# Optimization experiments

Measured on AMD Instinct MI355X. Metric: run time of the kernel, lower is better.

The kernel has to match this reference:

```python
import jax, jax.numpy as jnp
import numpy as np

PH, CH, Z, H, W, NK = 4, 8, 8, 320, 320, 4096
ITERS, GAMMA, TAU, EPS, RATIO = 3, 0.1, 0.2, 0.01, 0.2
LO, HI = int(Z * RATIO), Z - int(Z * RATIO)  # effective_slice = slice(1, 7)
TWO_PI = 2.0 * np.pi


def to_c(x):
    return jax.lax.complex(x[..., 0], x[..., 1])


def warp(img, flow):
    # MVF motion warp. img: (PH, Z, H, W) complex; flow: (PH, 2, Z, H, W) pixel displacements.
    gy = jnp.clip(jnp.arange(H, dtype=flow.dtype)[:, None] + flow[:, 0], 0.0, H - 1.0)
    gx = jnp.clip(jnp.arange(W, dtype=flow.dtype)[None, :] + flow[:, 1], 0.0, W - 1.0)
    y0 = jnp.floor(gy); x0 = jnp.floor(gx)
    wy = gy - y0; wx = gx - x0
    y0 = y0.astype(jnp.int32); x0 = x0.astype(jnp.int32)
    y1 = jnp.minimum(y0 + 1, H - 1); x1 = jnp.minimum(x0 + 1, W - 1)
    flat = img.reshape(PH, Z, H * W)
    def g(yi, xi):
        return jnp.take_along_axis(flat, (yi * W + xi).reshape(PH, Z, H * W), axis=-1).reshape(PH, Z, H, W)
    return (g(y0, x0) * ((1 - wy) * (1 - wx)) + g(y0, x1) * ((1 - wy) * wx)
            + g(y1, x0) * (wy * (1 - wx)) + g(y1, x1) * (wy * wx))


def nufft(img, traj):
    # Type-2 NUFFT via FFT + bilinear k-space interpolation.
    # img: (PH, CH, Z, H, W) complex; traj: (PH, 2, NK) in [-pi, pi).
    F = jnp.fft.fftshift(jnp.fft.fft2(img), axes=(-2, -1))
    gy = jnp.clip((traj[:, 0] / TWO_PI + 0.5) * H, 0.0, H - 1.0)
    gx = jnp.clip((traj[:, 1] / TWO_PI + 0.5) * W, 0.0, W - 1.0)
    def samp(Fp, gyp, gxp):
        y0 = jnp.floor(gyp); x0 = jnp.floor(gxp)
        wy = gyp - y0; wx = gxp - x0
        y0 = y0.astype(jnp.int32); x0 = x0.astype(jnp.int32)
        y1 = jnp.minimum(y0 + 1, H - 1); x1 = jnp.minimum(x0 + 1, W - 1)
        return (Fp[..., y0, x0] * ((1 - wy) * (1 - wx)) + Fp[..., y0, x1] * ((1 - wy) * wx)
                + Fp[..., y1, x0] * (wy * (1 - wx)) + Fp[..., y1, x1] * (wy * wx))
    return jax.vmap(samp)(F, gy, gx)  # (PH, CH, Z, NK)


def forward_model(x, mvf, csm_c, traj):
    # A = NUFFT * CSM * MVF
    warped = warp(x, mvf)                # (PH, Z, H, W)
    coil = csm_c[None] * warped[:, None]  # (PH, CH, Z, H, W)
    return nufft(coil, traj)             # (PH, CH, Z, NK)


def tv_energy(x):
    # smooth (anisotropic) TV energy; grad_reg = std * d/dx TV(x) = x_eff - regularization(x_eff)
    dy = x[..., 1:, :] - x[..., :-1, :]
    dx = x[..., :, 1:] - x[..., :, :-1]
    return jnp.sum(jnp.sqrt(jnp.abs(dy) ** 2 + 1e-8)) + jnp.sum(jnp.sqrt(jnp.abs(dx) ** 2 + 1e-8))


def setup_inputs():
    key = jax.random.key(0)
    ks = jax.random.split(key, 6)
    kspace_data = 0.1 * jax.random.normal(ks[0], (1, PH, CH, Z, NK, 2), jnp.float32)
    kspace_traj = jax.random.uniform(ks[1], (PH, 2, NK), jnp.float32, -np.pi, np.pi)
    image_init = jax.random.normal(ks[2], (1, PH, Z, H, W, 2), jnp.float32)
    mvf = 2.0 * jax.random.normal(ks[3], (PH, 2, Z, H, W), jnp.float32)
    csm = jax.random.normal(ks[4], (CH, Z, H, W, 2), jnp.float32) / np.sqrt(CH)
    std = jax.random.uniform(ks[5], (1,), jnp.float32, 0.05, 0.15)
    return {"kspace_data": kspace_data, "kspace_traj": kspace_traj, "image_init": image_init,
            "mvf": mvf, "csm": csm, "std": std}


def reference(kspace_data, kspace_traj, image_init, mvf, csm, std):
    y = to_c(kspace_data)[0]                   # (PH, CH, Z, NK)
    x = to_c(jnp.nan_to_num(image_init))[0]     # (PH, Z, H, W)
    csm_c = to_c(csm)                           # (CH, Z, H, W)
    s = std[0]

    def dc_loss(xv):
        est = forward_model(xv, mvf, csm_c, kspace_traj)[:, :, LO:HI]
        det = jax.lax.stop_gradient(jnp.abs(est))
        w = 1.0 / (det / det.max() + EPS)
        d = w * (est - y[:, :, LO:HI])
        # MSE over view_as_real = mean of squared real components
        return 0.5 * (jnp.mean(d.real ** 2) + jnp.mean(d.imag ** 2))

    for _ in range(ITERS):
        g_dc = jax.grad(dc_loss)(x)
        g_tv = s * jax.grad(tv_energy)(x[:, LO:HI])
        g_reg = jnp.zeros_like(x).at[:, LO:HI].set(g_tv)
        x = x - (GAMMA * g_dc + TAU * g_reg)
    return jnp.stack([x.real, x.imag], axis=-1)[None]  # (1, PH, Z, H, W, 2)
```

## Files before the change

kernel.cpp:

```cpp
#include <hip/hip_runtime.h>
#include <math.h>

#define PH   4
#define CHN  8
#define ZT   8
#define ZE   6
#define HG   320
#define WG   320
#define HW2  102400
#define NKP  4096
#define LSTR 321
#define FBCAP 131072u

constexpr float GAMMA_C = 0.1f;
constexpr float TAU_C   = 0.2f;
constexpr float EPS_C   = 0.01f;
constexpr float INV_N   = 1.0f / 786432.0f;
#define TWO_PI_F 6.28318530717958647692f

constexpr float W5R[5] = { 1.f,  0.30901699f, -0.80901699f, -0.80901699f,  0.30901699f};
constexpr float W5I[5] = { 0.f, -0.95105652f, -0.58778525f,  0.58778525f,  0.95105652f};

__device__ __forceinline__ float2 cmul(float2 a, float2 b){
  return make_float2(a.x*b.x - a.y*b.y, a.x*b.y + a.y*b.x);
}
__device__ __forceinline__ void cmac(float2& d, float2 a, float2 b){
  d.x = fmaf(a.x, b.x, fmaf(-a.y, b.y, d.x));
  d.y = fmaf(a.x, b.y, fmaf( a.y, b.x, d.y));
}

__device__ __forceinline__ void corners(float gy, float gx, int& y0, int& x0, int& y1, int& x1,
                                        float& w00, float& w01, float& w10, float& w11){
  float y0f = floorf(gy), x0f = floorf(gx);
  float wy = gy - y0f, wx = gx - x0f;
  y0 = (int)y0f; x0 = (int)x0f;
  y1 = min(y0 + 1, HG - 1); x1 = min(x0 + 1, WG - 1);
  w00 = (1.f - wy) * (1.f - wx);
  w01 = (1.f - wy) * wx;
  w10 = wy * (1.f - wx);
  w11 = wy * wx;
}

__device__ __forceinline__ void traj_to_grid(float ty, float tx, float& gy, float& gx){
  gy = fminf(fmaxf((ty / TWO_PI_F + 0.5f) * 320.f, 0.f), 319.f);
  gx = fminf(fmaxf((tx / TWO_PI_F + 0.5f) * 320.f, 0.f), 319.f);
}

struct FT {
  float2 t1, t2, t3, t4;
  float2 tw0, tw1, tw2, tw3, tw4;
  int br5, lane;
};

__device__ __forceinline__ FT ft_init(){
  FT f; int l = (int)(threadIdx.x & 63); f.lane = l;
  sincosf(-TWO_PI_F * (float)l * (1.0f/320.0f), &f.t1.y, &f.t1.x);
  f.t2 = cmul(f.t1, f.t1); f.t3 = cmul(f.t2, f.t1); f.t4 = cmul(f.t2, f.t2);
  sincosf(-TWO_PI_F * (float)(l & 31) * (1.0f/64.0f), &f.tw0.y, &f.tw0.x);
  sincosf(-TWO_PI_F * (float)(l & 15) * (1.0f/32.0f), &f.tw1.y, &f.tw1.x);
  sincosf(-TWO_PI_F * (float)(l &  7) * (1.0f/16.0f), &f.tw2.y, &f.tw2.x);
  sincosf(-TWO_PI_F * (float)(l &  3) * (1.0f/ 8.0f), &f.tw3.y, &f.tw3.x);
  f.tw4 = (l & 1) ? make_float2(0.f, -1.f) : make_float2(1.f, 0.f);
  int br = ((l&1)<<5) | ((l&2)<<3) | ((l&4)<<1) | ((l&8)>>1) | ((l&16)>>3) | ((l&32)>>5);
  f.br5 = 5 * br;
  return f;
}

template<int H>
__device__ __forceinline__ void bfly(float2& v, float2 tw, int lane){
  float px = __shfl_xor(v.x, H, 64);
  float py = __shfl_xor(v.y, H, 64);
  bool up = (lane & H) != 0;
  float ax = up ? px : v.x, ay = up ? py : v.y;
  float bx = up ? v.x : px, by = up ? v.y : py;
  float dx = ax - bx,  dy = ay - by;
  float mx = fmaf(dx, tw.x, -dy * tw.y);
  float my = fmaf(dx, tw.y,  dy * tw.x);
  v.x = up ? mx : (ax + bx);
  v.y = up ? my : (ay + by);
}

__device__ __forceinline__ void fft320w(const float2 a[5], const FT& f, float2* __restrict__ seg){
  float2 z[5];
  #pragma unroll
  for (int r = 0; r < 5; r++){
    float2 acc = a[0];
    #pragma unroll
    for (int q = 1; q < 5; q++){
      const int j = (q * r) % 5;
      cmac(acc, a[q], make_float2(W5R[j], W5I[j]));
    }
    z[r] = acc;
  }
  z[1] = cmul(z[1], f.t1); z[2] = cmul(z[2], f.t2);
  z[3] = cmul(z[3], f.t3); z[4] = cmul(z[4], f.t4);
  #pragma unroll
  for (int r = 0; r < 5; r++){
    float2 v = z[r];
    bfly<32>(v, f.tw0, f.lane);
    bfly<16>(v, f.tw1, f.lane);
    bfly< 8>(v, f.tw2, f.lane);
    bfly< 4>(v, f.tw3, f.lane);
    bfly< 2>(v, f.tw4, f.lane);
    {
      float px = __shfl_xor(v.x, 1, 64);
      float py = __shfl_xor(v.y, 1, 64);
      bool up = (f.lane & 1) != 0;
      float ax = up ? px : v.x, ay = up ? py : v.y;
      float bx = up ? v.x : px, by = up ? v.y : py;
      v.x = up ? (ax - bx) : (ax + bx);
      v.y = up ? (ay - by) : (ay + by);
    }
    seg[f.br5 + r] = v;
  }
}

__global__ __launch_bounds__(256) void k_khist(const float* __restrict__ traj, unsigned* __restrict__ xhist){
  int gid = blockIdx.x * 256 + threadIdx.x;
  if (gid >= PH * NKP) return;
  int p = gid >> 12, k = gid & (NKP - 1);
  float gy, gx;
  traj_to_grid(traj[(p * 2 + 0) * NKP + k], traj[(p * 2 + 1) * NKP + k], gy, gx);
  atomicAdd(&xhist[p * WG + (int)floorf(gx)], 1u);
}

__global__ void k_kscan(const unsigned* __restrict__ xhist, unsigned* __restrict__ xcur,
                        unsigned* __restrict__ xbnd){
  int p = threadIdx.x;
  if (p < PH){
    unsigned acc = 0;
    for (int b = 0; b < WG; b++){ xcur[p * WG + b] = acc; xbnd[p * (WG + 1) + b] = acc; acc += xhist[p * WG + b]; }
    xbnd[p * (WG + 1) + WG] = acc;
  }
}

__global__ __launch_bounds__(256) void k_kperm(const float* __restrict__ traj, unsigned* __restrict__ xcur,
                                               float4* __restrict__ permx){
  int gid = blockIdx.x * 256 + threadIdx.x;
  if (gid >= PH * NKP) return;
  int p = gid >> 12, k = gid & (NKP - 1);
  float gy, gx;
  traj_to_grid(traj[(p * 2 + 0) * NKP + k], traj[(p * 2 + 1) * NKP + k], gy, gx);
  unsigned sx = atomicAdd(&xcur[p * WG + (int)floorf(gx)], 1u);
  permx[p * NKP + sx] = make_float4(__uint_as_float((unsigned)k), gy, gx, 0.f);
}

__global__ __launch_bounds__(256) void k_init(const float2* __restrict__ img0, float2* __restrict__ x, int n){
  int i = blockIdx.x * 256 + threadIdx.x;
  if (i < n){
    float2 v = img0[i];
    v.x = isnan(v.x) ? 0.f : fminf(fmaxf(v.x, -3.4028235e38f), 3.4028235e38f);
    v.y = isnan(v.y) ? 0.f : fminf(fmaxf(v.y, -3.4028235e38f), 3.4028235e38f);
    x[i] = v;
  }
}

__global__ __launch_bounds__(256) void k_warp_tv(const float2* __restrict__ x, const float* __restrict__ mvf,
                                                 float2* __restrict__ warped, float2* __restrict__ gtv){
  int gid = blockIdx.x * 256 + threadIdx.x;
  int hw = gid % HW2;
  int pz = gid / HW2;
  int zz = pz % ZE, p = pz / ZE, z = zz + 1;
  int h = hw / WG, w = hw - h * WG;
  const float* mv = mvf + ((size_t)(p * 2 + 0) * ZT + z) * HW2;
  float fy = mv[hw];
  float fx = mv[(size_t)ZT * HW2 + hw];
  float gy = fminf(fmaxf((float)h + fy, 0.f), 319.f);
  float gx = fminf(fmaxf((float)w + fx, 0.f), 319.f);
  int y0, x0, y1, x1; float w00, w01, w10, w11;
  corners(gy, gx, y0, x0, y1, x1, w00, w01, w10, w11);
  const float2* xs = x + (size_t)(p * ZT + z) * HW2;
  float2 v00 = xs[y0 * WG + x0], v01 = xs[y0 * WG + x1];
  float2 v10 = xs[y1 * WG + x0], v11 = xs[y1 * WG + x1];
  float2 o;
  o.x = v00.x * w00 + v01.x * w01 + v10.x * w10 + v11.x * w11;
  o.y = v00.y * w00 + v01.y * w01 + v10.y * w10 + v11.y * w11;
  warped[gid] = o;
  float2 xc = xs[hw];
  float tre = 0.f, tim = 0.f;
  if (h > 0){
    float2 n = xs[hw - WG];
    float dr = xc.x - n.x, di = xc.y - n.y;
    float r = sqrtf(dr * dr + di * di + 1e-8f);
    tre += dr / r; tim += di / r;
  }
  if (h < HG - 1){
    float2 n = xs[hw + WG];
    float dr = n.x - xc.x, di = n.y - xc.y;
    float r = sqrtf(dr * dr + di * di + 1e-8f);
    tre -= dr / r; tim -= di / r;
  }
  if (w > 0){
    float2 n = xs[hw - 1];
    float dr = xc.x - n.x, di = xc.y - n.y;
    float r = sqrtf(dr * dr + di * di + 1e-8f);
    tre += dr / r; tim += di / r;
  }
  if (w < WG - 1){
    float2 n = xs[hw + 1];
    float dr = n.x - xc.x, di = n.y - xc.y;
    float r = sqrtf(dr * dr + di * di + 1e-8f);
    tre -= dr / r; tim -= di / r;
  }
  gtv[gid] = make_float2(tre, -tim);
}

__global__ __launch_bounds__(512) void k_fft_row_fwd(const float2* __restrict__ warped, const float2* __restrict__ csm,
                                                     float2* __restrict__ FT_, int p0){
  __shared__ float2 seg[8 * LSTR];
  FT f = ft_init();
  int wid = threadIdx.x >> 6, l = f.lane;
  int hg = blockIdx.x % 40; int sl = blockIdx.x / 40;
  int zz = sl % ZE; int s2 = sl / ZE; int c = s2 % CHN; int pp = s2 / CHN;
  int p = p0 + pp; int z = zz + 1;
  int h = hg * 8 + wid;
  const float2* wr = warped + ((size_t)(p * ZE + zz)) * HW2 + (size_t)h * WG;
  const float2* cs = csm + ((size_t)(c * ZT + z)) * HW2 + (size_t)h * WG;
  float sgn = ((h + l) & 1) ? -1.f : 1.f;
  float2 a[5];
  #pragma unroll
  for (int q = 0; q < 5; q++){
    float2 v = cmul(wr[64 * q + l], cs[64 * q + l]);
    a[q] = make_float2(v.x * sgn, v.y * sgn);
  }
  fft320w(a, f, seg + wid * LSTR);
  __syncthreads();
  float2* out = FT_ + (size_t)sl * HW2 + hg * 8;
  for (int i = threadIdx.x; i < 8 * WG; i += 512){
    int w = i >> 3; int hh = i & 7;
    out[(size_t)w * HG + hh] = seg[hh * LSTR + w];
  }
}

__global__ __launch_bounds__(256) void k_fft_col_sample(const float2* __restrict__ FT_, const float4* __restrict__ permx,
                                                        const unsigned* __restrict__ xbnd, float2* __restrict__ est,
                                                        unsigned int* __restrict__ dmax, int p0){
  __shared__ float2 seg[9 * LSTR];
  FT f = ft_init();
  int tid = threadIdx.x; int wid = tid >> 6, l = f.lane;
  int cg = blockIdx.x % 40; int sl = blockIdx.x / 40;
  int s2 = sl / ZE; int pp = s2 / CHN;
  int p = p0 + pp;
  int cbase = cg * 8;
  const int ncol = (cbase + 8 <= WG - 1) ? 9 : 8;
  const float2* Fs = FT_ + (size_t)sl * HW2 + (size_t)cbase * HG;
  #pragma unroll
  for (int cc = 0; cc < 3; cc++){
    int col = cc * 4 + wid;
    if (col < ncol){
      const float2* src = Fs + (size_t)col * HG;
      float2 a[5];
      #pragma unroll
      for (int q = 0; q < 5; q++) a[q] = src[64 * q + l];
      fft320w(a, f, seg + col * LSTR);
    }
  }
  __syncthreads();
  int lo = (int)xbnd[p * (WG + 1) + cbase];
  int hi = (int)xbnd[p * (WG + 1) + min(cbase + 8, WG)];
  float2* eb = est + ((size_t)(p0 * CHN * ZE) + sl) * NKP;
  const float4* px = permx + p * NKP;
  float md2 = 0.f;
  for (int j = lo + tid; j < hi; j += 256){
    float4 e4 = px[j];
    int y0, x0, y1, x1; float w00, w01, w10, w11;
    corners(e4.y, e4.z, y0, x0, y1, x1, w00, w01, w10, w11);
    int lc0 = x0 - cbase, lc1 = x1 - cbase;
    float2 v00 = seg[lc0 * LSTR + y0], v01 = seg[lc1 * LSTR + y0];
    float2 v10 = seg[lc0 * LSTR + y1], v11 = seg[lc1 * LSTR + y1];
    float2 e;
    e.x = v00.x * w00 + v01.x * w01 + v10.x * w10 + v11.x * w11;
    e.y = v00.y * w00 + v01.y * w01 + v10.y * w10 + v11.y * w11;
    eb[j] = e;
    md2 = fmaxf(md2, e.x * e.x + e.y * e.y);
  }
  for (int off = 32; off > 0; off >>= 1) md2 = fmaxf(md2, __shfl_down(md2, off, 64));
  if ((tid & 63) == 0 && md2 > 0.f) atomicMax(dmax, __float_as_uint(md2));
}

__global__ __launch_bounds__(256) void k_weights(float2* __restrict__ est, const float2* __restrict__ kdata,
                                                 const float4* __restrict__ permx,
                                                 const unsigned int* __restrict__ dmax){
  int gid = blockIdx.x * 256 + threadIdx.x;
  int j = gid & (NKP - 1);
  int t = gid >> 12;
  int zz = t % ZE; int pc = t / ZE; int z = zz + 1;
  int p = pc / CHN;
  int k = (int)__float_as_uint(permx[p * NKP + j].x);
  float md = sqrtf(__uint_as_float(*dmax));
  float2 e = est[gid];
  float det = sqrtf(e.x * e.x + e.y * e.y);
  float wv = 1.0f / (det / md + EPS_C);
  float sc = wv * wv * INV_N;
  float2 y = kdata[((size_t)pc * ZT + z) * NKP + k];
  est[gid] = make_float2(sc * (e.x - y.x), -sc * (e.y - y.y));
}

__global__ __launch_bounds__(256) void k_fft_col_scatter(const float2* __restrict__ G, const float4* __restrict__ permx,
                                                         const unsigned* __restrict__ xbnd,
                                                         float2* __restrict__ F, int p0){
  __shared__ float2 ld[16 * LSTR];
  FT f = ft_init();
  int tid = threadIdx.x; int wid = tid >> 6, l = f.lane;
  int cg = blockIdx.x % 20; int sl = blockIdx.x / 20;
  int s2 = sl / ZE; int pp = s2 / CHN;
  int p = p0 + pp;
  for (int i = tid; i < 16 * LSTR; i += 256) ld[i] = make_float2(0.f, 0.f);
  __syncthreads();
  int cbase = cg * 16;
  int lo = (cbase > 0) ? (int)xbnd[p * (WG + 1) + cbase - 1] : 0;
  int hi = (int)xbnd[p * (WG + 1) + min(cbase + 16, WG)];
  const float2* Gs = G + ((size_t)(p0 * CHN * ZE) + sl) * NKP;
  const float4* px = permx + p * NKP;
  for (int j = lo + tid; j < hi; j += 256){
    float4 e4 = px[j];
    int y0, x0, y1, x1; float w00, w01, w10, w11;
    corners(e4.y, e4.z, y0, x0, y1, x1, w00, w01, w10, w11);
    float2 gv = Gs[j];
    int c0 = x0 - cbase, c1 = x1 - cbase;
    if ((unsigned)c0 < 16u){
      atomicAdd(&ld[c0 * LSTR + y0].x, gv.x * w00); atomicAdd(&ld[c0 * LSTR + y0].y, gv.y * w00);
      atomicAdd(&ld[c0 * LSTR + y1].x, gv.x * w10); atomicAdd(&ld[c0 * LSTR + y1].y, gv.y * w10);
    }
    if ((unsigned)c1 < 16u){
      atomicAdd(&ld[c1 * LSTR + y0].x, gv.x * w01); atomicAdd(&ld[c1 * LSTR + y0].y, gv.y * w01);
      atomicAdd(&ld[c1 * LSTR + y1].x, gv.x * w11); atomicAdd(&ld[c1 * LSTR + y1].y, gv.y * w11);
    }
  }
  __syncthreads();
  #pragma unroll
  for (int cc = 0; cc < 4; cc++){
    float2* base = ld + (wid * 4 + cc) * LSTR;
    float2 a[5];
    #pragma unroll
    for (int q = 0; q < 5; q++) a[q] = base[64 * q + l];
    fft320w(a, f, base);
  }
  __syncthreads();
  float2* Fs = F + (size_t)sl * HW2 + cbase;
  for (int i = tid; i < 5120; i += 256){ int h = i >> 4, col = i & 15; Fs[h * WG + col] = ld[col * LSTR + h]; }
}

__global__ __launch_bounds__(512) void k_fft_row_bwd(const float2* __restrict__ F, const float2* __restrict__ csm,
                                                     float2* __restrict__ gwarped, int p0){
  __shared__ float2 seg[8 * LSTR];
  FT f = ft_init();
  int tid = threadIdx.x; int c = tid >> 6, l = f.lane;
  int bid = blockIdx.x;
  int h = bid % HG; int b2 = bid / HG;
  int zz = b2 % ZE; int pp = b2 / ZE;
  int p = p0 + pp; int z = zz + 1;
  const float2* Fl = F + ((size_t)((pp * CHN + c) * ZE + zz)) * HW2 + (size_t)h * WG;
  float2 a[5];
  #pragma unroll
  for (int q = 0; q < 5; q++) a[q] = Fl[64 * q + l];
  fft320w(a, f, seg + c * LSTR);
  __syncthreads();
  if (tid < WG){
    int w = tid;
    float2 acc = make_float2(0.f, 0.f);
    #pragma unroll
    for (int cc = 0; cc < 8; cc++){
      cmac(acc, seg[cc * LSTR + w], csm[((size_t)(cc * ZT + z)) * HW2 + (size_t)h * WG + w]);
    }
    float sg = ((h + w) & 1) ? -1.f : 1.f;
    gwarped[((size_t)(p * ZE + zz)) * HW2 + (size_t)h * WG + w] = make_float2(acc.x * sg, acc.y * sg);
  }
}

#define TRG 8
#define HAG 8
__global__ __launch_bounds__(512) void k_warpadj_update(const float2* __restrict__ gw, const float* __restrict__ mvf,
                                                        const float2* __restrict__ gtv, const float* __restrict__ stdp,
                                                        float2* __restrict__ x,
                                                        uint4* __restrict__ fb, unsigned int* __restrict__ fbcnt){
  __shared__ float lt[TRG * WG * 2];
  int tid = threadIdx.x;
  int bid = blockIdx.x;
  int tile = bid % 40; int pz = bid / 40;
  int zz = pz % ZE, p = pz / ZE, z = zz + 1;
  int R = tile * TRG;
  for (int i = tid; i < TRG * WG * 2; i += 512) lt[i] = 0.f;
  __syncthreads();
  const float* mvy = mvf + ((size_t)(p * 2 + 0) * ZT + z) * HW2;
  const float* mvx = mvy + (size_t)ZT * HW2;
  const float2* g = gw + (size_t)pz * HW2;
  const size_t xbase = (size_t)(p * ZT + z) * HW2;
  int wlo = max(R - HAG, 0), whi = min(R + TRG + HAG, HG);
  int npx = (whi - wlo) * WG;
  int base0 = wlo * WG;
  int i = tid;
  float fy = 0.f, fx = 0.f; float2 gv = make_float2(0.f, 0.f);
  if (i < npx){ fy = mvy[base0 + i]; fx = mvx[base0 + i]; gv = g[base0 + i]; }
  while (i < npx){
    int inx = i + 512;
    float fy2 = 0.f, fx2 = 0.f; float2 gv2 = make_float2(0.f, 0.f);
    if (inx < npx){ fy2 = mvy[base0 + inx]; fx2 = mvx[base0 + inx]; gv2 = g[base0 + inx]; }
    int hh = i / WG; int w = i - hh * WG;
    int h = wlo + hh;
    float gy = fminf(fmaxf((float)h + fy, 0.f), 319.f);
    float gx = fminf(fmaxf((float)w + fx, 0.f), 319.f);
    int y0, x0, y1, x1; float w00, w01, w10, w11;
    corners(gy, gx, y0, x0, y1, x1, w00, w01, w10, w11);
    bool owner = (h >= R) && (h < R + TRG);
    #define PROC(Y, XC, WT) { \
      int ry = (Y) - R; \
      if ((unsigned)ry < (unsigned)TRG){ \
        atomicAdd(&lt[(ry * WG + (XC)) * 2 + 0], gv.x * (WT)); \
        atomicAdd(&lt[(ry * WG + (XC)) * 2 + 1], gv.y * (WT)); \
      } else if (owner){ \
        int Ry = (Y) & ~(TRG - 1); \
        if (h < Ry - HAG || h >= Ry + TRG + HAG){ \
          unsigned slot = atomicAdd(fbcnt, 1u); \
          if (slot < FBCAP) fb[slot] = make_uint4((unsigned)(xbase + (size_t)(Y) * WG + (XC)), \
                                                  __float_as_uint(gv.x * (WT)), __float_as_uint(gv.y * (WT)), 0u); \
        } \
      } \
    }
    PROC(y0, x0, w00); PROC(y0, x1, w01); PROC(y1, x0, w10); PROC(y1, x1, w11);
    #undef PROC
    i = inx; fy = fy2; fx = fx2; gv = gv2;
  }
  __syncthreads();
  float s = stdp[0];
  const float2* gt = gtv + (size_t)pz * HW2;
  for (int i2 = tid; i2 < TRG * WG; i2 += 512){
    int yy = i2 / WG; int w = i2 - yy * WG;
    int hw = (R + yy) * WG + w;
    float2 xv = x[xbase + hw];
    float2 tv = gt[hw];
    xv.x -= GAMMA_C * lt[i2 * 2 + 0] + TAU_C * s * tv.x;
    xv.y -= GAMMA_C * lt[i2 * 2 + 1] + TAU_C * s * tv.y;
    x[xbase + hw] = xv;
  }
}

__global__ __launch_bounds__(256) void k_fixup(const uint4* __restrict__ fb, const unsigned int* __restrict__ fbcnt,
                                               float2* __restrict__ x){
  unsigned n = *fbcnt; if (n > FBCAP) n = FBCAP;
  for (unsigned i = blockIdx.x * 256 + threadIdx.x; i < n; i += gridDim.x * 256){
    uint4 e = fb[i];
    atomicAdd(&x[e.x].x, -GAMMA_C * __uint_as_float(e.y));
    atomicAdd(&x[e.x].y, -GAMMA_C * __uint_as_float(e.z));
  }
}

extern "C" void kernel_launch(void* const* d_in, const int* in_sizes, int n_in,
                              void* d_out, int out_size, void* d_ws, size_t ws_size,
                              hipStream_t stream) {
  const float2* kdata = (const float2*)d_in[0];
  const float*  traj  = (const float*) d_in[1];
  const float2* img0  = (const float2*)d_in[2];
  const float*  mvf   = (const float*) d_in[3];
  const float2* csm   = (const float2*)d_in[4];
  const float*  stdp  = (const float*) d_in[5];
  float2* x = (float2*)d_out;

  const size_t F_B  = (size_t)CHN * ZE * HW2 * 8;
  const size_t W_B  = (size_t)PH * ZE * HW2 * 8;
  const size_t E_B  = (size_t)PH * CHN * ZE * NKP * 8;
  const size_t FB_B = (size_t)FBCAP * 16;
  const size_t P_B  = (size_t)PH * NKP * 16;
  const size_t SORT_B = P_B + 4 * 8192;

  size_t need_big = 4 * F_B + 2 * W_B + E_B + 512 + FB_B + SORT_B;
  const int NP = (ws_size >= need_big) ? 4 : 1;

  char* cur = (char*)d_ws;
  float2* F      = (float2*)cur;  cur += (size_t)NP * F_B;
  float2* warped = (float2*)cur;  cur += W_B;
  float2* est    = (float2*)cur;  cur += E_B;
  float2* gtvb   = (float2*)cur;  cur += W_B;
  unsigned int* dmax  = (unsigned int*)cur; cur += 128;
  unsigned int* fbcnt = (unsigned int*)cur; cur += 128;
  uint4* fb           = (uint4*)cur;        cur += FB_B;
  float4* permx       = (float4*)cur;       cur += P_B;
  unsigned* xhist     = (unsigned*)cur;     cur += 8192;
  unsigned* xcur      = (unsigned*)cur;     cur += 8192;
  unsigned* xbnd      = (unsigned*)cur;     cur += 8192;

  k_init<<<12800, 256, 0, stream>>>(img0, x, PH * ZT * HW2);
  hipMemsetAsync(xhist, 0, 8192, stream);
  k_khist<<<64, 256, 0, stream>>>(traj, xhist);
  k_kscan<<<1, 64, 0, stream>>>(xhist, xcur, xbnd);
  k_kperm<<<64, 256, 0, stream>>>(traj, xcur, permx);

  for (int it = 0; it < 3; it++){
    k_warp_tv<<<9600, 256, 0, stream>>>(x, mvf, warped, gtvb);
    hipMemsetAsync(dmax, 0, 4, stream);
    for (int p0 = 0; p0 < PH; p0 += NP){
      k_fft_row_fwd   <<<NP * 1920, 512, 0, stream>>>(warped, csm, F, p0);
      k_fft_col_sample<<<NP * 1920, 256, 0, stream>>>(F, permx, xbnd, est, dmax, p0);
    }
    k_weights<<<3072, 256, 0, stream>>>(est, kdata, permx, dmax);
    for (int p0 = 0; p0 < PH; p0 += NP){
      k_fft_col_scatter<<<NP *  960, 256, 0, stream>>>(est, permx, xbnd, F, p0);
      k_fft_row_bwd    <<<NP * 1920, 512, 0, stream>>>(F, csm, warped, p0);
    }
    hipMemsetAsync(fbcnt, 0, 4, stream);
    k_warpadj_update<<<960, 512, 0, stream>>>(warped, mvf, gtvb, stdp, x, fb, fbcnt);
    k_fixup<<<16, 256, 0, stream>>>(fb, fbcnt, x);
  }
}
```

Baseline: 1.795 ms.

## Fuse DC weighting into column scatter, fold memsets into warp kernel, batch column loads

Removes the separate k_weights pass by computing the residual weighting inside k_fft_col_scatter for each sample, and moves the dmax/fbcnt zeroing into k_warp_tv so two memset launches go away. The column-sample kernel now issues all global loads for its three columns before running the FFTs, to overlap memory latency. The trade-off is recomputing weights in overlapping boundary ranges of the scatter, extra register pressure from holding 15 float2 values, and relying on launch ordering for the in-kernel counter reset.

```diff
diff --git a/kernel.cpp b/kernel.cpp
--- a/kernel.cpp
+++ b/kernel.cpp
@@ -156,7 +156,9 @@
 }
 
 __global__ __launch_bounds__(256) void k_warp_tv(const float2* __restrict__ x, const float* __restrict__ mvf,
-                                                 float2* __restrict__ warped, float2* __restrict__ gtv){
+                                                 float2* __restrict__ warped, float2* __restrict__ gtv,
+                                                 unsigned int* __restrict__ dmax, unsigned int* __restrict__ fbcnt){
+  if (blockIdx.x == 0 && threadIdx.x == 0){ *dmax = 0u; *fbcnt = 0u; }
   int gid = blockIdx.x * 256 + threadIdx.x;
   int hw = gid % HW2;
   int pz = gid / HW2;
@@ -244,16 +246,20 @@
   int cbase = cg * 8;
   const int ncol = (cbase + 8 <= WG - 1) ? 9 : 8;
   const float2* Fs = FT_ + (size_t)sl * HW2 + (size_t)cbase * HG;
+  float2 areg[3][5];
   #pragma unroll
   for (int cc = 0; cc < 3; cc++){
     int col = cc * 4 + wid;
     if (col < ncol){
       const float2* src = Fs + (size_t)col * HG;
-      float2 a[5];
       #pragma unroll
-      for (int q = 0; q < 5; q++) a[q] = src[64 * q + l];
-      fft320w(a, f, seg + col * LSTR);
-    }
+      for (int q = 0; q < 5; q++) areg[cc][q] = src[64 * q + l];
+    }
+  }
+  #pragma unroll
+  for (int cc = 0; cc < 3; cc++){
+    int col = cc * 4 + wid;
+    if (col < ncol) fft320w(areg[cc], f, seg + col * LSTR);
   }
   __syncthreads();
   int lo = (int)xbnd[p * (WG + 1) + cbase];
@@ -278,45 +284,37 @@
   if ((tid & 63) == 0 && md2 > 0.f) atomicMax(dmax, __float_as_uint(md2));
 }
 
-__global__ __launch_bounds__(256) void k_weights(float2* __restrict__ est, const float2* __restrict__ kdata,
-                                                 const float4* __restrict__ permx,
-                                                 const unsigned int* __restrict__ dmax){
-  int gid = blockIdx.x * 256 + threadIdx.x;
-  int j = gid & (NKP - 1);
-  int t = gid >> 12;
-  int zz = t % ZE; int pc = t / ZE; int z = zz + 1;
-  int p = pc / CHN;
-  int k = (int)__float_as_uint(permx[p * NKP + j].x);
-  float md = sqrtf(__uint_as_float(*dmax));
-  float2 e = est[gid];
-  float det = sqrtf(e.x * e.x + e.y * e.y);
-  float wv = 1.0f / (det / md + EPS_C);
-  float sc = wv * wv * INV_N;
-  float2 y = kdata[((size_t)pc * ZT + z) * NKP + k];
-  est[gid] = make_float2(sc * (e.x - y.x), -sc * (e.y - y.y));
-}
-
-__global__ __launch_bounds__(256) void k_fft_col_scatter(const float2* __restrict__ G, const float4* __restrict__ permx,
+__global__ __launch_bounds__(256) void k_fft_col_scatter(const float2* __restrict__ est, const float2* __restrict__ kdata,
+                                                         const float4* __restrict__ permx,
                                                          const unsigned* __restrict__ xbnd,
+                                                         const unsigned int* __restrict__ dmax,
                                                          float2* __restrict__ F, int p0){
   __shared__ float2 ld[16 * LSTR];
   FT f = ft_init();
   int tid = threadIdx.x; int wid = tid >> 6, l = f.lane;
   int cg = blockIdx.x % 20; int sl = blockIdx.x / 20;
-  int s2 = sl / ZE; int pp = s2 / CHN;
-  int p = p0 + pp;
+  int zz = sl % ZE; int s2 = sl / ZE; int c = s2 % CHN; int pp = s2 / CHN;
+  int p = p0 + pp; int z = zz + 1;
   for (int i = tid; i < 16 * LSTR; i += 256) ld[i] = make_float2(0.f, 0.f);
   __syncthreads();
+  float md = sqrtf(__uint_as_float(*dmax));
   int cbase = cg * 16;
   int lo = (cbase > 0) ? (int)xbnd[p * (WG + 1) + cbase - 1] : 0;
   int hi = (int)xbnd[p * (WG + 1) + min(cbase + 16, WG)];
-  const float2* Gs = G + ((size_t)(p0 * CHN * ZE) + sl) * NKP;
+  const float2* Es = est + ((size_t)(p0 * CHN * ZE) + sl) * NKP;
+  const float2* kd = kdata + ((size_t)(p * CHN + c) * ZT + z) * NKP;
   const float4* px = permx + p * NKP;
   for (int j = lo + tid; j < hi; j += 256){
     float4 e4 = px[j];
+    int k = (int)__float_as_uint(e4.x);
     int y0, x0, y1, x1; float w00, w01, w10, w11;
     corners(e4.y, e4.z, y0, x0, y1, x1, w00, w01, w10, w11);
-    float2 gv = Gs[j];
+    float2 e = Es[j];
+    float det = sqrtf(e.x * e.x + e.y * e.y);
+    float wv = 1.0f / (det / md + EPS_C);
+    float sc = wv * wv * INV_N;
+    float2 y = kd[k];
+    float2 gv = make_float2(sc * (e.x - y.x), -sc * (e.y - y.y));
     int c0 = x0 - cbase, c1 = x1 - cbase;
     if ((unsigned)c0 < 16u){
       atomicAdd(&ld[c0 * LSTR + y0].x, gv.x * w00); atomicAdd(&ld[c0 * LSTR + y0].y, gv.y * w00);
@@ -486,18 +484,15 @@
   k_kperm<<<64, 256, 0, stream>>>(traj, xcur, permx);
 
   for (int it = 0; it < 3; it++){
-    k_warp_tv<<<9600, 256, 0, stream>>>(x, mvf, warped, gtvb);
-    hipMemsetAsync(dmax, 0, 4, stream);
+    k_warp_tv<<<9600, 256, 0, stream>>>(x, mvf, warped, gtvb, dmax, fbcnt);
     for (int p0 = 0; p0 < PH; p0 += NP){
       k_fft_row_fwd   <<<NP * 1920, 512, 0, stream>>>(warped, csm, F, p0);
       k_fft_col_sample<<<NP * 1920, 256, 0, stream>>>(F, permx, xbnd, est, dmax, p0);
     }
-    k_weights<<<3072, 256, 0, stream>>>(est, kdata, permx, dmax);
     for (int p0 = 0; p0 < PH; p0 += NP){
-      k_fft_col_scatter<<<NP *  960, 256, 0, stream>>>(est, permx, xbnd, F, p0);
+      k_fft_col_scatter<<<NP *  960, 256, 0, stream>>>(est, kdata, permx, xbnd, dmax, F, p0);
       k_fft_row_bwd    <<<NP * 1920, 512, 0, stream>>>(F, csm, warped, p0);
     }
-    hipMemsetAsync(fbcnt, 0, 4, stream);
     k_warpadj_update<<<960, 512, 0, stream>>>(warped, mvf, gtvb, stdp, x, fb, fbcnt);
     k_fixup<<<16, 256, 0, stream>>>(fb, fbcnt, x);
   }
```

Result: no change. 1.775 ms (-1.1%).
